# Kernel optimization log

Measured on AMD Instinct MI355X. Metric: run time of the kernel, lower is better.

## Reference

```python
import jax, jax.numpy as jnp
import numpy as np

B, S, D, F, E, K, R, H = 4, 1024, 1024, 512, 8, 2, 64, 256
TEMP = 1.0          # step=0 -> 0.5+0.5*cos(0)=1.0, clamp(min=0.1) -> 1.0
BW, EW, ZW = 0.3, 0.1, 1e-4


def fq(t):
    """Per-tensor symmetric int8 fake-quant with straight-through estimator."""
    s = jnp.maximum(jnp.max(jnp.abs(t)) / 127.0, 1e-8)
    q = jnp.clip(jnp.round(t / s), -128, 127) * s
    return t + jax.lax.stop_gradient(q - t)


def lora_lin(h, W, A, Bm):
    # base weight is frozen (requires_grad=False) and fake-quantized
    y = h @ fq(jax.lax.stop_gradient(W)).T + (h @ Bm.T) @ A.T
    return fq(y)


def ffn(h, w1, a1, b1, w2, a2, b2, w3, a3, b3):
    # use_swiglu=True path: gate = sigmoid(w3(x)); out = w2(w1(x)*gate); dropout=eval identity
    gate = jax.nn.sigmoid(lora_lin(h, w3, a3, b3))
    out = lora_lin(lora_lin(h, w1, a1, b1) * gate, w2, a2, b2)
    return fq(out)


def setup_inputs() -> dict:
    key = jax.random.key(0)
    k = jax.random.split(key, 32)
    n = lambda i, shp: jax.random.normal(k[i], shp, dtype=jnp.float32) * 0.02
    return {
        "x": jax.random.normal(k[0], (B, S, D), dtype=jnp.float32),
        "scorer_w": n(1, (E, D)), "scorer_b": jnp.zeros((E,), jnp.float32),
        "p1_w": n(2, (H, D)), "p1_b": jnp.zeros((H,), jnp.float32),
        "p2_w": n(3, (E, H)), "p2_b": jnp.zeros((E,), jnp.float32),
        "ew1_w": n(4, (E, F, D)), "ew1_a": n(5, (E, F, R)), "ew1_b": n(6, (E, R, D)),
        "ew2_w": n(7, (E, D, F)), "ew2_a": n(8, (E, D, R)), "ew2_b": n(9, (E, R, F)),
        "ew3_w": n(10, (E, F, D)), "ew3_a": n(11, (E, F, R)), "ew3_b": n(12, (E, R, D)),
        "s1_w": n(13, (F, D)), "s1_a": n(14, (F, R)), "s1_b": n(15, (R, D)),
        "s2_w": n(16, (D, F)), "s2_a": n(17, (D, R)), "s2_b": n(18, (R, F)),
        "s3_w": n(19, (F, D)), "s3_a": n(20, (F, R)), "s3_b": n(21, (R, D)),
    }


def reference(x, scorer_w, scorer_b, p1_w, p1_b, p2_w, p2_b,
              ew1_w, ew1_a, ew1_b, ew2_w, ew2_a, ew2_b, ew3_w, ew3_a, ew3_b,
              s1_w, s1_a, s1_b, s2_w, s2_a, s2_b, s3_w, s3_a, s3_b):
    xf = x.reshape(-1, D)                                           # [T, D]
    # --- router (per-token) ---
    base = (xf @ scorer_w.T + scorer_b) / TEMP                      # [T, E]
    policy = jax.nn.softmax(jax.nn.relu(xf @ p1_w.T + p1_b) @ p2_w.T + p2_b, axis=-1)
    scores = jax.nn.softmax((base + policy) * 0.5, axis=-1)         # fp32 softmax
    entropy = -(scores * jnp.log(scores + 1e-6)).sum(-1).mean()
    z_loss = ZW * (jax.nn.logsumexp(base, axis=-1) ** 2).mean()
    weights, indices = jax.lax.top_k(scores, K)                     # [T, K]
    weights = weights * TEMP
    cw = (jax.nn.one_hot(indices, E, dtype=weights.dtype) * weights[..., None]).sum(1)  # [T, E]
    usage = cw.sum(0)                                               # [E]
    uf = usage / (usage.mean() + 1e-6)
    balance_loss = BW * jnp.var(uf, ddof=1) - EW * entropy + z_loss
    # --- expert dispatch: dense masked combine (faithful to weighted scatter-add) ---
    eout = jax.vmap(lambda w1, a1, b1, w2, a2, b2, w3, a3, b3:
                    ffn(xf, w1, a1, b1, w2, a2, b2, w3, a3, b3))(
        ew1_w, ew1_a, ew1_b, ew2_w, ew2_a, ew2_b, ew3_w, ew3_a, ew3_b)  # [E, T, D]
    y = jnp.einsum('te,etd->td', cw, eout)                          # weighted combine
    z = ffn(xf, s1_w, s1_a, s1_b, s2_w, s2_a, s2_b, s3_w, s3_a, s3_b)
    out = (y + z).reshape(x.shape)
    return (out, usage, balance_loss, jnp.float32(0.0), jnp.float32(0.0))
```

## Files before the change

### kernel.cpp

```cpp
#include <hip/hip_runtime.h>

#define TTOK 4096
#define DDIM 1024
#define FDIM 512
#define NEXP 8
#define HDIM 256
#define RLORA 64
#define CROWS 14336

using u16 = unsigned short;
using f4v = __attribute__((ext_vector_type(4))) float;
using bfrag = __attribute__((ext_vector_type(8))) short;
using u16x8 = __attribute__((ext_vector_type(8))) unsigned short;

static __device__ __forceinline__ float bf2f(u16 u) {
  union { unsigned int u; float f; } x; x.u = ((unsigned int)u) << 16; return x.f;
}
static __device__ __forceinline__ u16 f2bf(float f) {
  union { float f; unsigned int u; } x; x.f = f;
  unsigned int r = (x.u + 0x7fffu + ((x.u >> 16) & 1u)) >> 16;
  return (u16)r;
}
static __device__ __forceinline__ float fq1(float t, float s) {
  float q = rintf(t / s);
  q = fminf(fmaxf(q, -128.f), 127.f);
  return q * s;
}

struct GemmGArgs {
  const u16* A; const u16* B; u16* C;
  const int* tokmap; const int2* blkmap; const int* nbrow;
};

#define STAGE1(d, kt, h) \
  __builtin_amdgcn_global_load_lds( \
    (const __attribute__((address_space(1))) void*)(gs[h] + (size_t)(kt)*64), \
    (__attribute__((address_space(3))) void*)&lds[(d)*32768 + (h)*8192 + tid*8], \
    16, 0, 0)

template <int MODE>
__global__ __launch_bounds__(1024, 4) void gemm256g(GemmGArgs g) {
  const int bid = blockIdx.x;
  const int logical = (bid & 7) * 28 + (bid >> 3);
  const int br = logical >> 2;
  if (br >= g.nbrow[0]) return;
  const int2 bm = g.blkmap[br];
  const int e = bm.x;
  const int m0 = bm.y;
  const int n0 = (logical & 3) * 256;
  const int tid = threadIdx.x;
  const int lane = tid & 63;
  const int wave = tid >> 6;
  const int wr = wave >> 2;
  const int wc = wave & 3;

  constexpr int K = MODE ? 1024 : 512;
  const u16* Bp = g.B + (size_t)e * (MODE ? 1048576 : 524288);

  __shared__ u16 lds[65536];

  const u16* gs[4];
#pragma unroll
  for (int h = 0; h < 4; h++) {
    const int row = tid >> 3, p = tid & 7;
    const int glog = p ^ (row & 7);
    const u16* basep;
    if (h < 2) {
      const int grow = m0 + h * 128 + row;
      const int t = MODE ? g.tokmap[grow] : grow;
      basep = g.A + (size_t)t * K;
    } else {
      basep = Bp + (size_t)(n0 + (h - 2) * 128 + row) * K;
    }
    gs[h] = basep + glog * 8;
  }

  f4v acc[4][4];
#pragma unroll
  for (int i = 0; i < 4; i++)
#pragma unroll
    for (int j = 0; j < 4; j++) acc[i][j] = (f4v){0.f, 0.f, 0.f, 0.f};

  const int q = lane >> 4;
  const int lx = lane & 7;
  const int l15 = lane & 15;

#pragma unroll
  for (int h = 0; h < 4; h++) STAGE1(0, 0, h);
  __syncthreads();

  constexpr int nt = K >> 6;
  for (int kt = 0; kt < nt; ++kt) {
    const int d = kt & 1;
    const int dn = d ^ 1;
    const bool more = (kt + 1 < nt);
#pragma unroll
    for (int kk = 0; kk < 2; ++kk) {
      if (more) {
        if (kk == 0) { STAGE1(dn, kt + 1, 0); STAGE1(dn, kt + 1, 1); }
        else         { STAGE1(dn, kt + 1, 2); STAGE1(dn, kt + 1, 3); }
      }
      bfrag afr[4], bfr[4];
      const int pa = ((kk * 4 + q) ^ lx) << 3;
      const int abase = d * 32768 + (wr >> 1) * 8192 + (((wr & 1) << 6) + l15) * 64 + pa;
#pragma unroll
      for (int mi = 0; mi < 4; mi++) afr[mi] = *(const bfrag*)&lds[abase + mi * 1024];
      const int bbase = d * 32768 + (2 + (wc >> 1)) * 8192 + (((wc & 1) << 6) + l15) * 64 + pa;
#pragma unroll
      for (int ni = 0; ni < 4; ni++) bfr[ni] = *(const bfrag*)&lds[bbase + ni * 1024];
      __builtin_amdgcn_s_setprio(1);
#pragma unroll
      for (int mi = 0; mi < 4; mi++)
#pragma unroll
        for (int ni = 0; ni < 4; ni++)
          acc[mi][ni] = __builtin_amdgcn_mfma_f32_16x16x32_bf16(afr[mi], bfr[ni], acc[mi][ni], 0, 0, 0);
      __builtin_amdgcn_s_setprio(0);
    }
    __syncthreads();
  }

  const int crow0 = m0 + wr * 64 + q * 4;

  if (MODE == 1) {
    u16* stage = lds;
    const int lrow0 = wr * 64 + q * 4;
    if (wc >= 2) {
      const int lc = (wc - 2) * 64 + l15;
#pragma unroll
      for (int mi = 0; mi < 4; mi++)
#pragma unroll
        for (int ni = 0; ni < 4; ni++)
#pragma unroll
          for (int r = 0; r < 4; r++)
            stage[(lrow0 + mi * 16 + r) * 136 + lc + ni * 16] = f2bf(acc[mi][ni][r]);
    }
    __syncthreads();
    if (wc < 2) {
      const int lc = wc * 64 + l15;
      const int fbase = (n0 >> 1) + lc;
#pragma unroll
      for (int mi = 0; mi < 4; mi++)
#pragma unroll
        for (int r = 0; r < 4; r++) {
          const int rowg = crow0 + mi * 16 + r;
          const int lr = lrow0 + mi * 16 + r;
#pragma unroll
          for (int ni = 0; ni < 4; ni++) {
            float y1 = acc[mi][ni][r];
            float y3 = bf2f(stage[lr * 136 + lc + ni * 16]);
            float h = y1 / (1.f + __expf(-y3));
            g.C[(size_t)rowg * FDIM + fbase + ni * 16] = f2bf(h);
          }
        }
    }
  } else {
    const int ccol0 = n0 + wc * 64 + l15;
#pragma unroll
    for (int mi = 0; mi < 4; mi++)
#pragma unroll
      for (int ni = 0; ni < 4; ni++) {
        const int col = ccol0 + ni * 16;
#pragma unroll
        for (int r = 0; r < 4; r++)
          g.C[(size_t)(crow0 + mi * 16 + r) * 1024 + col] = f2bf(acc[mi][ni][r]);
      }
  }
}

struct MidArgs {
  const u16* A64; const u16* B64; u16* C64; const float* bias64;
  const u16* A0; const u16* B0;
  const u16* Wb;
  u16* C13; u16* C2e;
  const float* amaxP;
};

__global__ __launch_bounds__(256) void mid_kernel(MidArgs g) {
  __shared__ u16 smem[25600];
  __shared__ float s_sw;
  const int bid = blockIdx.x;
  const int tid = threadIdx.x;
  const int lane = tid & 63;
  const int wave = tid >> 6;

  if (bid < 256) {
    const int wr = wave >> 1, wc = wave & 1;
    const int m0 = (bid & 63) * 64, n0 = (bid >> 6) * 64;
    const int K = DDIM, N = HDIM;
    u16* As = smem;
    u16* Bs = smem + 2048;

    const int ldrow = tid >> 2;
    const int swzcol = (((tid & 3) ^ ((tid >> 3) & 3)) << 3);
    const u16* ga = g.A64 + (size_t)(m0 + ldrow) * K + swzcol;
    const u16* gb = g.B64 + (size_t)(n0 + ldrow) * K + swzcol;

    f4v acc[2][2];
#pragma unroll
    for (int i = 0; i < 2; i++)
#pragma unroll
      for (int j = 0; j < 2; j++) acc[i][j] = (f4v){0.f, 0.f, 0.f, 0.f};

    const int rbase = lane & 15;
    const int q = lane >> 4;
    const int pg = (q ^ ((rbase >> 1) & 3)) << 3;
    const int arow = (wr << 5) + rbase;
    const int brow = (wc << 5) + rbase;

    for (int kt = 0; kt < K; kt += 32) {
      __builtin_amdgcn_global_load_lds((const __attribute__((address_space(1))) void*)(ga),
          (__attribute__((address_space(3))) void*)&As[tid * 8], 16, 0, 0);
      __builtin_amdgcn_global_load_lds((const __attribute__((address_space(1))) void*)(gb),
          (__attribute__((address_space(3))) void*)&Bs[tid * 8], 16, 0, 0);
      ga += 32; gb += 32;
      __syncthreads();
      bfrag af[2], bf[2];
#pragma unroll
      for (int mi = 0; mi < 2; mi++)
        af[mi] = *(const bfrag*)&As[(arow + mi * 16) * 32 + pg];
#pragma unroll
      for (int ni = 0; ni < 2; ni++)
        bf[ni] = *(const bfrag*)&Bs[(brow + ni * 16) * 32 + pg];
#pragma unroll
      for (int mi = 0; mi < 2; mi++)
#pragma unroll
        for (int ni = 0; ni < 2; ni++)
          acc[mi][ni] = __builtin_amdgcn_mfma_f32_16x16x32_bf16(af[mi], bf[ni], acc[mi][ni], 0, 0, 0);
      __syncthreads();
    }

    const int crow0 = m0 + (wr << 5) + ((lane >> 4) << 2);
    const int ccol0 = n0 + (wc << 5) + (lane & 15);
#pragma unroll
    for (int mi = 0; mi < 2; mi++)
#pragma unroll
      for (int ni = 0; ni < 2; ni++) {
        const int n = ccol0 + ni * 16;
        const float b = g.bias64[n];
#pragma unroll
        for (int r = 0; r < 4; r++) {
          float v = fmaxf(acc[mi][ni][r] + b, 0.f);
          g.C64[(size_t)(crow0 + mi * 16 + r) * N + n] = f2bf(v);
        }
      }
    return;
  }

  const int fid = bid - 256;
  const int z = fid >> 6;
  const int rem = fid & 63;
  const int bx = rem & 7, by = rem >> 3;
  const bool is13 = z < 18;
  if (is13 ? (bx >= 4) : (by >= 4)) return;
  const int N = is13 ? 1024 : 512;
  const int K = 64;
  const u16* Ap = is13 ? g.A0 + (size_t)z * 32768 : g.A0 + 589824 + (size_t)(z - 18) * 65536;
  const u16* Bp = is13 ? g.B0 + (size_t)z * 65536 : g.B0 + 1179648 + (size_t)(z - 18) * 32768;
  const u16* Wf = g.Wb + (size_t)z * 524288;
  u16* Cb; int flag;
  if (is13) {
    const int slot = (z >= 16) ? 8 : (z & 7);
    Cb = g.C13 + (size_t)slot * 1048576;
    flag = (z >= 8 && z < 16) || z == 17 ? 2 : 1;
  } else {
    Cb = g.C2e + (size_t)(z - 18) * 524288;
    flag = 0;
  }

  const int wr = wave >> 1, wc = wave & 1;
  const int m0 = bx * 128, n0 = by * 128;
  u16* As = smem;
  u16* Bs = smem + 4096;
  u16* stage = smem + 8192;

  if (wave == 0) {
    float m = fmaxf(g.amaxP[z * 128 + lane], g.amaxP[z * 128 + 64 + lane]);
#pragma unroll
    for (int off = 32; off > 0; off >>= 1) m = fmaxf(m, __shfl_xor(m, off));
    if (lane == 0) s_sw = fmaxf(m / 127.f, 1e-8f);
  }

  const int ldrow = tid >> 2;
  const int swzcol = (((tid & 3) ^ ((tid >> 3) & 3)) << 3);
  const u16* ga = Ap + (size_t)(m0 + ldrow) * K + swzcol;
  const u16* gb = Bp + (size_t)(n0 + ldrow) * K + swzcol;
  const size_t rowstep = (size_t)64 * K;

  f4v acc[4][4];
#pragma unroll
  for (int i = 0; i < 4; i++)
#pragma unroll
    for (int j = 0; j < 4; j++) acc[i][j] = (f4v){0.f, 0.f, 0.f, 0.f};

  const int rbase = lane & 15;
  const int q = lane >> 4;
  const int pg = (q ^ ((rbase >> 1) & 3)) << 3;
  const int arow = (wr << 6) + rbase;
  const int brow = (wc << 6) + rbase;

  for (int kt = 0; kt < K; kt += 32) {
    __builtin_amdgcn_global_load_lds((const __attribute__((address_space(1))) void*)(ga),
        (__attribute__((address_space(3))) void*)&As[tid * 8], 16, 0, 0);
    __builtin_amdgcn_global_load_lds((const __attribute__((address_space(1))) void*)(ga + rowstep),
        (__attribute__((address_space(3))) void*)&As[(256 + tid) * 8], 16, 0, 0);
    __builtin_amdgcn_global_load_lds((const __attribute__((address_space(1))) void*)(gb),
        (__attribute__((address_space(3))) void*)&Bs[tid * 8], 16, 0, 0);
    __builtin_amdgcn_global_load_lds((const __attribute__((address_space(1))) void*)(gb + rowstep),
        (__attribute__((address_space(3))) void*)&Bs[(256 + tid) * 8], 16, 0, 0);
    ga += 32; gb += 32;
    __syncthreads();
    bfrag af[4], bf[4];
#pragma unroll
    for (int mi = 0; mi < 4; mi++)
      af[mi] = *(const bfrag*)&As[(arow + mi * 16) * 32 + pg];
#pragma unroll
    for (int ni = 0; ni < 4; ni++)
      bf[ni] = *(const bfrag*)&Bs[(brow + ni * 16) * 32 + pg];
#pragma unroll
    for (int mi = 0; mi < 4; mi++)
#pragma unroll
      for (int ni = 0; ni < 4; ni++)
        acc[mi][ni] = __builtin_amdgcn_mfma_f32_16x16x32_bf16(af[mi], bf[ni], acc[mi][ni], 0, 0, 0);
    __syncthreads();
  }

  const int lrow0 = (wr << 6) + ((lane >> 4) << 2);
  const int lcol0 = (wc << 6) + (lane & 15);
#pragma unroll
  for (int mi = 0; mi < 4; mi++)
#pragma unroll
    for (int ni = 0; ni < 4; ni++) {
      const int n = lcol0 + ni * 16;
#pragma unroll
      for (int r = 0; r < 4; r++)
        stage[(lrow0 + mi * 16 + r) * 136 + n] = f2bf(acc[mi][ni][r]);
    }
  __syncthreads();
  const float sw = s_sw;

  const int dm0 = flag ? (((m0 >> 7) << 8) + (flag == 2 ? 128 : 0)) : m0;
#pragma unroll
  for (int j = 0; j < 8; j++) {
    const int s = j * 256 + tid;
    const int lr = s >> 4;
    const int n8 = (s & 15) << 3;
    const u16x8 wv = *(const u16x8*)&Wf[(size_t)(m0 + lr) * N + n0 + n8];
    const bfrag sv = *(const bfrag*)&stage[lr * 136 + n8];
    u16x8 o;
#pragma unroll
    for (int k = 0; k < 8; k++)
      o[k] = f2bf(fq1(bf2f(wv[k]), sw) + bf2f((u16)sv[k]));
    *(u16x8*)&Cb[(size_t)(dm0 + lr) * N + n0 + n8] = o;
  }
}

struct PrepArgs {
  const float* W[27]; u16* Wraw; float* amaxP;
  const float* xf; u16* xfb;
  const float* p1w; u16* p1wb;
  const float* Asrc[27]; u16* Adst;
  const float* Bsrc[27]; u16* Bdst;
};
__global__ __launch_bounds__(256) void prep_kernel(PrepArgs a) {
  const int bid = blockIdx.x;
  const int tid = threadIdx.x;
  if (bid < 3456) {
    const int t = bid >> 7;
    const int bx = bid & 127;
    const float4* src = (const float4*)a.W[t];
    ushort4* dst = (ushort4*)(a.Wraw + (size_t)t * 524288);
    const int i0 = bx * 256 + tid;
    float4 v0 = src[i0];
    float4 v1 = src[i0 + 32768];
    float4 v2 = src[i0 + 65536];
    float4 v3 = src[i0 + 98304];
    ushort4 o0, o1, o2, o3;
    o0.x = f2bf(v0.x); o0.y = f2bf(v0.y); o0.z = f2bf(v0.z); o0.w = f2bf(v0.w);
    o1.x = f2bf(v1.x); o1.y = f2bf(v1.y); o1.z = f2bf(v1.z); o1.w = f2bf(v1.w);
    o2.x = f2bf(v2.x); o2.y = f2bf(v2.y); o2.z = f2bf(v2.z); o2.w = f2bf(v2.w);
    o3.x = f2bf(v3.x); o3.y = f2bf(v3.y); o3.z = f2bf(v3.z); o3.w = f2bf(v3.w);
    dst[i0] = o0; dst[i0 + 32768] = o1; dst[i0 + 65536] = o2; dst[i0 + 98304] = o3;
    float m01 = fmaxf(fmaxf(fabsf(v0.x), fabsf(v0.y)), fmaxf(fabsf(v0.z), fabsf(v0.w)));
    float m11 = fmaxf(fmaxf(fabsf(v1.x), fabsf(v1.y)), fmaxf(fabsf(v1.z), fabsf(v1.w)));
    float m21 = fmaxf(fmaxf(fabsf(v2.x), fabsf(v2.y)), fmaxf(fabsf(v2.z), fabsf(v2.w)));
    float m31 = fmaxf(fmaxf(fabsf(v3.x), fabsf(v3.y)), fmaxf(fabsf(v3.z), fabsf(v3.w)));
    float lmax = fmaxf(fmaxf(m01, m11), fmaxf(m21, m31));
#pragma unroll
    for (int off = 32; off > 0; off >>= 1) lmax = fmaxf(lmax, __shfl_xor(lmax, off));
    __shared__ float wm[4];
    if ((tid & 63) == 0) wm[tid >> 6] = lmax;
    __syncthreads();
    if (tid == 0)
      a.amaxP[t * 128 + bx] = fmaxf(fmaxf(wm[0], wm[1]), fmaxf(wm[2], wm[3]));
    return;
  }
  const int cid = bid - 3456;
  const int slice = cid >> 10;
  const int g0 = (cid & 1023) * 256 + tid;
  const int stride = 262144;
  if (slice == 0) {
    for (int i = g0; i < 1048576; i += stride) {
      float4 v = ((const float4*)a.xf)[i];
      ushort4 o; o.x = f2bf(v.x); o.y = f2bf(v.y); o.z = f2bf(v.z); o.w = f2bf(v.w);
      ((ushort4*)a.xfb)[i] = o;
    }
  } else if (slice == 1) {
    for (int i = g0; i < 65536; i += stride) {
      float4 v = ((const float4*)a.p1w)[i];
      ushort4 o; o.x = f2bf(v.x); o.y = f2bf(v.y); o.z = f2bf(v.z); o.w = f2bf(v.w);
      ((ushort4*)a.p1wb)[i] = o;
    }
  } else if (slice == 2) {
    for (int i = g0; i < 1179648; i += stride) {
      int t, off;
      if (i < 589824) { t = i >> 15; off = i & 32767; }
      else { int j = i - 589824; t = 18 + (j >> 16); off = j & 65535; }
      a.Adst[i] = f2bf(a.Asrc[t][off]);
    }
  } else {
    for (int i = g0; i < 1474560; i += stride) {
      int t, src;
      if (i < 1179648) { t = i >> 16; int off = i & 65535; src = (off & 63) * 1024 + (off >> 6); }
      else { int j = i - 1179648; t = 18 + (j >> 15); int off = j & 32767; src = (off & 63) * 512 + (off >> 6); }
      a.Bdst[i] = f2bf(a.Bsrc[t][src]);
    }
  }
}

struct RouterArgs {
  const float* xf; const u16* ph;
  const float* sw; const float* sb;
  const float* p2w; const float* p2b;
  int* idx2; float2* wb;
  float* partials;
  int* histArr;
};
__global__ __launch_bounds__(256) void router_kernel(RouterArgs a) {
  __shared__ float sw[8][1024];
  __shared__ float p2[8][256];
  __shared__ float blog[16][8];
  __shared__ float plog[16][8];
  __shared__ int hist[8];
  const int tid = threadIdx.x;
  {
    const float4* s0 = (const float4*)a.sw;
    float4* d0 = (float4*)&sw[0][0];
    for (int i = tid; i < 2048; i += 256) d0[i] = s0[i];
    const float4* s1 = (const float4*)a.p2w;
    float4* d1 = (float4*)&p2[0][0];
    for (int i = tid; i < 512; i += 256) d1[i] = s1[i];
  }
  if (tid < 8) hist[tid] = 0;
  __syncthreads();
  const int tl = tid >> 4, s = tid & 15;
  const int token = blockIdx.x * 16 + tl;
  {
    float acc[8] = {0,0,0,0,0,0,0,0}, pacc[8] = {0,0,0,0,0,0,0,0};
    const float4* xrow = (const float4*)(a.xf + (size_t)token * 1024);
    for (int i = 0; i < 16; i++) {
      const int d4 = i * 16 + s;
      float4 xv = xrow[d4];
#pragma unroll
      for (int e = 0; e < 8; e++) {
        float4 wv = ((const float4*)&sw[e][0])[d4];
        acc[e] += xv.x * wv.x + xv.y * wv.y + xv.z * wv.z + xv.w * wv.w;
      }
    }
    const u16* phrow = a.ph + (size_t)token * 256;
    for (int i = 0; i < 16; i++) {
      const int h = i * 16 + s;
      float pv = bf2f(phrow[h]);
#pragma unroll
      for (int e = 0; e < 8; e++) pacc[e] += pv * p2[e][h];
    }
#pragma unroll
    for (int off = 8; off > 0; off >>= 1)
#pragma unroll
      for (int e = 0; e < 8; e++) {
        acc[e] += __shfl_xor(acc[e], off);
        pacc[e] += __shfl_xor(pacc[e], off);
      }
    if (s == 0) {
#pragma unroll
      for (int e = 0; e < 8; e++) {
        blog[tl][e] = acc[e] + a.sb[e];
        plog[tl][e] = pacc[e] + a.p2b[e];
      }
    }
  }
  __syncthreads();

  float vals[10];
#pragma unroll
  for (int v = 0; v < 10; v++) vals[v] = 0.f;
  if (tid < 16) {
    const int tok = blockIdx.x * 16 + tid;
    float b[8], p[8];
#pragma unroll
    for (int e = 0; e < 8; e++) { b[e] = blog[tid][e]; p[e] = plog[tid][e]; }
    float pm = p[0];
#pragma unroll
    for (int e = 1; e < 8; e++) pm = fmaxf(pm, p[e]);
    float pe[8], psum = 0.f;
#pragma unroll
    for (int e = 0; e < 8; e++) { pe[e] = expf(p[e] - pm); psum += pe[e]; }
    const float pinv = 1.f / psum;
    float sl[8];
#pragma unroll
    for (int e = 0; e < 8; e++) sl[e] = (b[e] + pe[e] * pinv) * 0.5f;
    float sm = sl[0];
#pragma unroll
    for (int e = 1; e < 8; e++) sm = fmaxf(sm, sl[e]);
    float sc[8], ssum = 0.f;
#pragma unroll
    for (int e = 0; e < 8; e++) { sc[e] = expf(sl[e] - sm); ssum += sc[e]; }
    const float sinv = 1.f / ssum;
    float ent = 0.f;
#pragma unroll
    for (int e = 0; e < 8; e++) { float v = sc[e] * sinv; sc[e] = v; ent -= v * logf(v + 1e-6f); }
    float bm = b[0];
#pragma unroll
    for (int e = 1; e < 8; e++) bm = fmaxf(bm, b[e]);
    float zs = 0.f;
#pragma unroll
    for (int e = 0; e < 8; e++) zs += expf(b[e] - bm);
    const float lse = logf(zs) + bm;
    float m1 = -1e30f, m2 = -1e30f; int i1 = 0, i2 = 0;
#pragma unroll
    for (int e = 0; e < 8; e++) {
      float v = sc[e];
      if (v > m1) { m2 = m1; i2 = i1; m1 = v; i1 = e; }
      else if (v > m2) { m2 = v; i2 = e; }
    }
    a.idx2[tok] = i1 | (i2 << 8);
    a.wb[tok] = make_float2(m1, m2);
    atomicAdd(&hist[i1], 1);
    atomicAdd(&hist[i2], 1);
    vals[0] = ent; vals[1] = lse * lse;
    vals[2 + i1] = m1; vals[2 + i2] = m2;
  }
  if (tid < 64) {
#pragma unroll
    for (int v = 0; v < 10; v++)
#pragma unroll
      for (int off = 32; off > 0; off >>= 1) vals[v] += __shfl_down(vals[v], off);
    if (tid == 0)
#pragma unroll
      for (int v = 0; v < 10; v++) a.partials[blockIdx.x * 10 + v] = vals[v];
  }
  __syncthreads();
  if (tid < 8) a.histArr[blockIdx.x * 8 + tid] = hist[tid];
}

__global__ __launch_bounds__(256) void compact_setup(const int* idx2, const int* histArr,
                                                     int2* blkmap, int* nbrow, int* tokmap,
                                                     int* posb, const float* partials, float* tail) {
  const int e = blockIdx.x;
  const int tid = threadIdx.x;
  const int lane = tid & 63, wv = tid >> 6;
  __shared__ int scnt[8];
  __shared__ int wcnt[4][8];

  {
    int local[8];
#pragma unroll
    for (int i = 0; i < 8; i++) local[i] = histArr[tid * 8 + i];
#pragma unroll
    for (int i = 0; i < 8; i++) {
      int v = local[i];
#pragma unroll
      for (int off = 32; off > 0; off >>= 1) v += __shfl_down(v, off);
      if (lane == 0) wcnt[wv][i] = v;
    }
  }
  __syncthreads();
  if (tid < 8) scnt[tid] = wcnt[0][tid] + wcnt[1][tid] + wcnt[2][tid] + wcnt[3][tid];
  __syncthreads();

  if (e == 8) {
    __shared__ float wpart[4][10];
    float pv[10];
#pragma unroll
    for (int v = 0; v < 10; v++) pv[v] = partials[tid * 10 + v];
#pragma unroll
    for (int v = 0; v < 10; v++) {
      float t = pv[v];
#pragma unroll
      for (int off = 32; off > 0; off >>= 1) t += __shfl_down(t, off);
      if (lane == 0) wpart[wv][v] = t;
    }
    __syncthreads();
    if (tid == 0) {
      float pt[10];
#pragma unroll
      for (int v = 0; v < 10; v++)
        pt[v] = wpart[0][v] + wpart[1][v] + wpart[2][v] + wpart[3][v];
      const float ent = pt[0], z = pt[1];
      float us[8];
      for (int ex = 0; ex < 8; ex++) us[ex] = pt[2 + ex];
      float tot = 0.f;
      for (int ex = 0; ex < 8; ex++) tot += us[ex];
      const float meanu = tot / 8.f;
      float uf[8], mu = 0.f;
      for (int ex = 0; ex < 8; ex++) { uf[ex] = us[ex] / (meanu + 1e-6f); mu += uf[ex]; }
      mu /= 8.f;
      float var = 0.f;
      for (int ex = 0; ex < 8; ex++) { float d = uf[ex] - mu; var += d * d; }
      var /= 7.f;
      const float bl = 0.3f * var - 0.1f * (ent / 4096.f) + 1e-4f * (z / 4096.f);
      for (int ex = 0; ex < 8; ex++) tail[ex] = us[ex];
      tail[8] = bl; tail[9] = 0.f; tail[10] = 0.f;
      int o = 0, nb = 16;
      for (int i = 0; i < 16; i++) blkmap[i] = make_int2(8, i * 256);
      for (int ex = 0; ex < 8; ex++) {
        const int nbe = (scnt[ex] + 255) >> 8;
        for (int i = 0; i < nbe; i++) blkmap[nb++] = make_int2(ex, 4096 + o + i * 256);
        o += nbe << 8;
      }
      nbrow[0] = nb;
    }
    for (int t = tid; t < 4096; t += 256) tokmap[t] = t;
    return;
  }

  __shared__ int wtot[4];
  __shared__ int carry;
  if (tid == 0) carry = 0;
  __syncthreads();
  int off = 0;
  for (int i = 0; i < e; i++) off += ((scnt[i] + 255) >> 8) << 8;
  const int base = 4096 + off;
  for (int c = 0; c < 16; c++) {
    const int t = c * 256 + tid;
    const int ii = idx2[t];
    const int i1 = ii & 255, i2 = ii >> 8;
    const int flag = (i1 == e || i2 == e) ? 1 : 0;
    const unsigned long long m = __ballot(flag);
    const int pre = __popcll(m & ((1ull << lane) - 1ull));
    if (lane == 63) wtot[wv] = pre + flag;
    __syncthreads();
    int wbase = 0;
    for (int i = 0; i < wv; i++) wbase += wtot[i];
    if (flag) {
      const int row = base + carry + wbase + pre;
      tokmap[row] = t;
      posb[t * 2 + (i2 == e ? 1 : 0)] = row;
    }
    __syncthreads();
    if (tid == 0) carry += wtot[0] + wtot[1] + wtot[2] + wtot[3];
    __syncthreads();
  }
  const int ce = scnt[e];
  const int pend = ((ce + 255) >> 8) << 8;
  for (int r = ce + tid; r < pend; r += 256) tokmap[base + r] = 0;
}

__global__ __launch_bounds__(256) void combine_g(const u16* y2c, const int* posb,
                                                 const float2* wb, float* out) {
  const int t = blockIdx.x;
  const int c = threadIdx.x;
  const float2 w = wb[t];
  const int p1 = posb[t * 2], p2 = posb[t * 2 + 1];
  ushort4 s = ((const ushort4*)(y2c + (size_t)t * 1024))[c];
  ushort4 a = ((const ushort4*)(y2c + (size_t)p1 * 1024))[c];
  ushort4 b = ((const ushort4*)(y2c + (size_t)p2 * 1024))[c];
  float4 o;
  o.x = bf2f(s.x) + w.x * bf2f(a.x) + w.y * bf2f(b.x);
  o.y = bf2f(s.y) + w.x * bf2f(a.y) + w.y * bf2f(b.y);
  o.z = bf2f(s.z) + w.x * bf2f(a.z) + w.y * bf2f(b.z);
  o.w = bf2f(s.w) + w.x * bf2f(a.w) + w.y * bf2f(b.w);
  ((float4*)(out + (size_t)t * 1024))[c] = o;
}

extern "C" void kernel_launch(void* const* d_in, const int* in_sizes, int n_in,
                              void* d_out, int out_size, void* d_ws, size_t ws_size,
                              hipStream_t stream) {
  const float* x = (const float*)d_in[0];
  const float* scorer_w = (const float*)d_in[1];
  const float* scorer_b = (const float*)d_in[2];
  const float* p1_w = (const float*)d_in[3];
  const float* p1_b = (const float*)d_in[4];
  const float* p2_w = (const float*)d_in[5];
  const float* p2_b = (const float*)d_in[6];
  const float* ew1_w = (const float*)d_in[7];
  const float* ew1_a = (const float*)d_in[8];
  const float* ew1_b = (const float*)d_in[9];
  const float* ew2_w = (const float*)d_in[10];
  const float* ew2_a = (const float*)d_in[11];
  const float* ew2_b = (const float*)d_in[12];
  const float* ew3_w = (const float*)d_in[13];
  const float* ew3_a = (const float*)d_in[14];
  const float* ew3_b = (const float*)d_in[15];
  const float* s1_w = (const float*)d_in[16];
  const float* s1_a = (const float*)d_in[17];
  const float* s1_b = (const float*)d_in[18];
  const float* s2_w = (const float*)d_in[19];
  const float* s2_a = (const float*)d_in[20];
  const float* s2_b = (const float*)d_in[21];
  const float* s3_w = (const float*)d_in[22];
  const float* s3_a = (const float*)d_in[23];
  const float* s3_b = (const float*)d_in[24];
  float* outf = (float*)d_out;

  char* w = (char*)d_ws;
  auto alloc = [&](size_t bytes) { char* p = w; w += (bytes + 255) & ~(size_t)255; return p; };
  u16* xfb  = (u16*)alloc((size_t)TTOK * DDIM * 2);
  u16* ph   = (u16*)alloc((size_t)TTOK * HDIM * 2);
  u16* p1wb = (u16*)alloc((size_t)HDIM * DDIM * 2);
  u16* Adst = (u16*)alloc((size_t)1179648 * 2);
  u16* Bdst = (u16*)alloc((size_t)1474560 * 2);
  u16* Wraw = (u16*)alloc((size_t)27 * 524288 * 2);
  u16* W13  = (u16*)alloc((size_t)9 * 1024 * 1024 * 2);
  u16* W2e  = (u16*)alloc((size_t)9 * 1024 * 512 * 2);
  u16* h2c  = (u16*)alloc((size_t)CROWS * FDIM * 2);
  u16* y2c  = (u16*)alloc((size_t)CROWS * DDIM * 2);
  float* partials = (float*)alloc(256 * 10 * 4);
  float* amaxP = (float*)alloc(27 * 128 * 4);
  int* histArr = (int*)alloc(256 * 8 * 4);
  int2* blkmap = (int2*)alloc(64 * 8);
  int* nbrow  = (int*)alloc(4);
  int* tokmap = (int*)alloc(CROWS * 4);
  int* posb   = (int*)alloc(TTOK * 2 * 4);
  int* idx2   = (int*)alloc(TTOK * 4);
  float2* wb  = (float2*)alloc(TTOK * 8);

  {
    PrepArgs a{};
    for (int e = 0; e < 8; e++) {
      a.W[e] = ew1_w + (size_t)e * 524288;
      a.W[8 + e] = ew3_w + (size_t)e * 524288;
      a.W[18 + e] = ew2_w + (size_t)e * 524288;
      a.Asrc[e] = ew1_a + (size_t)e * 32768;
      a.Asrc[8 + e] = ew3_a + (size_t)e * 32768;
      a.Asrc[18 + e] = ew2_a + (size_t)e * 65536;
      a.Bsrc[e] = ew1_b + (size_t)e * 65536;
      a.Bsrc[8 + e] = ew3_b + (size_t)e * 65536;
      a.Bsrc[18 + e] = ew2_b + (size_t)e * 32768;
    }
    a.W[16] = s1_w; a.W[17] = s3_w; a.W[26] = s2_w;
    a.Asrc[16] = s1_a; a.Asrc[17] = s3_a; a.Asrc[26] = s2_a;
    a.Bsrc[16] = s1_b; a.Bsrc[17] = s3_b; a.Bsrc[26] = s2_b;
    a.Wraw = Wraw; a.amaxP = amaxP;
    a.xf = x; a.xfb = xfb; a.p1w = p1_w; a.p1wb = p1wb;
    a.Adst = Adst; a.Bdst = Bdst;
    hipLaunchKernelGGL(prep_kernel, dim3(7552), dim3(256), 0, stream, a);
  }
  {
    MidArgs g{};
    g.A64 = xfb; g.B64 = p1wb; g.C64 = ph; g.bias64 = p1_b;
    g.A0 = Adst; g.B0 = Bdst; g.Wb = Wraw; g.C13 = W13; g.C2e = W2e; g.amaxP = amaxP;
    hipLaunchKernelGGL(mid_kernel, dim3(1984), dim3(256), 0, stream, g);
  }
  {
    RouterArgs r{};
    r.xf = x; r.ph = ph; r.sw = scorer_w; r.sb = scorer_b;
    r.p2w = p2_w; r.p2b = p2_b;
    r.idx2 = idx2; r.wb = wb; r.partials = partials; r.histArr = histArr;
    hipLaunchKernelGGL(router_kernel, dim3(256), dim3(256), 0, stream, r);
  }
  hipLaunchKernelGGL(compact_setup, dim3(9), dim3(256), 0, stream,
                     idx2, histArr, blkmap, nbrow, tokmap, posb, partials,
                     outf + (size_t)TTOK * DDIM);
  {
    GemmGArgs g{xfb, W13, h2c, tokmap, blkmap, nbrow};
    hipLaunchKernelGGL(gemm256g<1>, dim3(224), dim3(1024), 0, stream, g);
  }
  {
    GemmGArgs g{h2c, W2e, y2c, tokmap, blkmap, nbrow};
    hipLaunchKernelGGL(gemm256g<0>, dim3(224), dim3(1024), 0, stream, g);
  }
  hipLaunchKernelGGL(combine_g, dim3(4096), dim3(256), 0, stream, y2c, posb, wb, outf);
}
```

Before: 147.5 us.

## Shrink grouped expert GEMM tiles from 256x256 to 128x128 for more blocks

Replaces the 1024-thread 256x256-tile grouped GEMM with a 256-thread 128x128-tile version, launching four times as many blocks so the 256 CUs get better occupancy and load balance. The W1/W3 interleaving produced by the mid kernel changes from 128-row to 64-row granularity so that each 128-column output tile still holds matching gate and up halves for the fused sigmoid epilogue. The cost is lower per-block data reuse and more global traffic for the A and B operands.

```diff
diff --git a/kernel.cpp b/kernel.cpp
--- a/kernel.cpp
+++ b/kernel.cpp
@@ -32,48 +32,52 @@
   const int* tokmap; const int2* blkmap; const int* nbrow;
 };
 
-#define STAGE1(d, kt, h) \
+#define STG(d, kt, h, l) \
   __builtin_amdgcn_global_load_lds( \
-    (const __attribute__((address_space(1))) void*)(gs[h] + (size_t)(kt)*64), \
-    (__attribute__((address_space(3))) void*)&lds[(d)*32768 + (h)*8192 + tid*8], \
+    (const __attribute__((address_space(1))) void*)(gs[(h)*4+(l)] + (size_t)(kt)*64), \
+    (__attribute__((address_space(3))) void*)&lds[(d)*16384 + (h)*8192 + (tid + (l)*256)*8], \
     16, 0, 0)
 
 template <int MODE>
-__global__ __launch_bounds__(1024, 4) void gemm256g(GemmGArgs g) {
+__global__ __launch_bounds__(256, 2) void gemm128g(GemmGArgs g) {
   const int bid = blockIdx.x;
-  const int logical = (bid & 7) * 28 + (bid >> 3);
-  const int br = logical >> 2;
+  const int logical = (bid & 7) * 112 + (bid >> 3);
+  const int br = logical >> 4;
   if (br >= g.nbrow[0]) return;
   const int2 bm = g.blkmap[br];
   const int e = bm.x;
-  const int m0 = bm.y;
-  const int n0 = (logical & 3) * 256;
+  const int sub = logical & 15;
+  const int m0 = bm.y + (sub >> 3) * 128;
+  const int n0 = (sub & 7) * 128;
   const int tid = threadIdx.x;
   const int lane = tid & 63;
   const int wave = tid >> 6;
-  const int wr = wave >> 2;
-  const int wc = wave & 3;
+  const int wr = wave >> 1;
+  const int wc = wave & 1;
 
   constexpr int K = MODE ? 1024 : 512;
   const u16* Bp = g.B + (size_t)e * (MODE ? 1048576 : 524288);
 
-  __shared__ u16 lds[65536];
-
-  const u16* gs[4];
-#pragma unroll
-  for (int h = 0; h < 4; h++) {
-    const int row = tid >> 3, p = tid & 7;
-    const int glog = p ^ (row & 7);
-    const u16* basep;
-    if (h < 2) {
-      const int grow = m0 + h * 128 + row;
-      const int t = MODE ? g.tokmap[grow] : grow;
-      basep = g.A + (size_t)t * K;
-    } else {
-      basep = Bp + (size_t)(n0 + (h - 2) * 128 + row) * K;
-    }
-    gs[h] = basep + glog * 8;
-  }
+  __shared__ u16 lds[32768];
+
+  const u16* gs[8];
+#pragma unroll
+  for (int h = 0; h < 2; h++)
+#pragma unroll
+    for (int l = 0; l < 4; l++) {
+      const int slot = tid + l * 256;
+      const int row = slot >> 3, p = slot & 7;
+      const int glog = p ^ (row & 7);
+      const u16* basep;
+      if (h == 0) {
+        const int grow = m0 + row;
+        const int t = MODE ? g.tokmap[grow] : grow;
+        basep = g.A + (size_t)t * K;
+      } else {
+        basep = Bp + (size_t)(n0 + row) * K;
+      }
+      gs[h * 4 + l] = basep + glog * 8;
+    }
 
   f4v acc[4][4];
 #pragma unroll
@@ -86,7 +90,9 @@
   const int l15 = lane & 15;
 
 #pragma unroll
-  for (int h = 0; h < 4; h++) STAGE1(0, 0, h);
+  for (int h = 0; h < 2; h++)
+#pragma unroll
+    for (int l = 0; l < 4; l++) STG(0, 0, h, l);
   __syncthreads();
 
   constexpr int nt = K >> 6;
@@ -97,15 +103,17 @@
 #pragma unroll
     for (int kk = 0; kk < 2; ++kk) {
       if (more) {
-        if (kk == 0) { STAGE1(dn, kt + 1, 0); STAGE1(dn, kt + 1, 1); }
-        else         { STAGE1(dn, kt + 1, 2); STAGE1(dn, kt + 1, 3); }
+        if (kk == 0) { STG(dn, kt + 1, 0, 0); STG(dn, kt + 1, 0, 1);
+                       STG(dn, kt + 1, 0, 2); STG(dn, kt + 1, 0, 3); }
+        else         { STG(dn, kt + 1, 1, 0); STG(dn, kt + 1, 1, 1);
+                       STG(dn, kt + 1, 1, 2); STG(dn, kt + 1, 1, 3); }
       }
       bfrag afr[4], bfr[4];
       const int pa = ((kk * 4 + q) ^ lx) << 3;
-      const int abase = d * 32768 + (wr >> 1) * 8192 + (((wr & 1) << 6) + l15) * 64 + pa;
+      const int abase = d * 16384 + (wr * 64 + l15) * 64 + pa;
 #pragma unroll
       for (int mi = 0; mi < 4; mi++) afr[mi] = *(const bfrag*)&lds[abase + mi * 1024];
-      const int bbase = d * 32768 + (2 + (wc >> 1)) * 8192 + (((wc & 1) << 6) + l15) * 64 + pa;
+      const int bbase = d * 16384 + 8192 + (wc * 64 + l15) * 64 + pa;
 #pragma unroll
       for (int ni = 0; ni < 4; ni++) bfr[ni] = *(const bfrag*)&lds[bbase + ni * 1024];
       __builtin_amdgcn_s_setprio(1);
@@ -120,24 +128,22 @@
   }
 
   const int crow0 = m0 + wr * 64 + q * 4;
+  const int lrow0 = wr * 64 + q * 4;
 
   if (MODE == 1) {
     u16* stage = lds;
-    const int lrow0 = wr * 64 + q * 4;
-    if (wc >= 2) {
-      const int lc = (wc - 2) * 64 + l15;
+    if (wc == 1) {
 #pragma unroll
       for (int mi = 0; mi < 4; mi++)
 #pragma unroll
         for (int ni = 0; ni < 4; ni++)
 #pragma unroll
           for (int r = 0; r < 4; r++)
-            stage[(lrow0 + mi * 16 + r) * 136 + lc + ni * 16] = f2bf(acc[mi][ni][r]);
-    }
-    __syncthreads();
-    if (wc < 2) {
-      const int lc = wc * 64 + l15;
-      const int fbase = (n0 >> 1) + lc;
+            stage[(lrow0 + mi * 16 + r) * 72 + ni * 16 + l15] = f2bf(acc[mi][ni][r]);
+    }
+    __syncthreads();
+    if (wc == 0) {
+      const int fbase = (n0 >> 1) + l15;
 #pragma unroll
       for (int mi = 0; mi < 4; mi++)
 #pragma unroll
@@ -147,7 +153,7 @@
 #pragma unroll
           for (int ni = 0; ni < 4; ni++) {
             float y1 = acc[mi][ni][r];
-            float y3 = bf2f(stage[lr * 136 + lc + ni * 16]);
+            float y3 = bf2f(stage[lr * 72 + ni * 16 + l15]);
             float h = y1 / (1.f + __expf(-y3));
             g.C[(size_t)rowg * FDIM + fbase + ni * 16] = f2bf(h);
           }
@@ -338,19 +344,20 @@
   __syncthreads();
   const float sw = s_sw;
 
-  const int dm0 = flag ? (((m0 >> 7) << 8) + (flag == 2 ? 128 : 0)) : m0;
 #pragma unroll
   for (int j = 0; j < 8; j++) {
     const int s = j * 256 + tid;
     const int lr = s >> 4;
     const int n8 = (s & 15) << 3;
-    const u16x8 wv = *(const u16x8*)&Wf[(size_t)(m0 + lr) * N + n0 + n8];
+    const int m = m0 + lr;
+    const int dm = flag ? (((m >> 6) << 7) + (m & 63) + (flag == 2 ? 64 : 0)) : m;
+    const u16x8 wv = *(const u16x8*)&Wf[(size_t)m * N + n0 + n8];
     const bfrag sv = *(const bfrag*)&stage[lr * 136 + n8];
     u16x8 o;
 #pragma unroll
     for (int k = 0; k < 8; k++)
       o[k] = f2bf(fq1(bf2f(wv[k]), sw) + bf2f((u16)sv[k]));
-    *(u16x8*)&Cb[(size_t)(dm0 + lr) * N + n0 + n8] = o;
+    *(u16x8*)&Cb[(size_t)dm * N + n0 + n8] = o;
   }
 }
 
@@ -763,11 +770,11 @@
                      outf + (size_t)TTOK * DDIM);
   {
     GemmGArgs g{xfb, W13, h2c, tokmap, blkmap, nbrow};
-    hipLaunchKernelGGL(gemm256g<1>, dim3(224), dim3(1024), 0, stream, g);
+    hipLaunchKernelGGL(gemm128g<1>, dim3(896), dim3(256), 0, stream, g);
   }
   {
     GemmGArgs g{h2c, W2e, y2c, tokmap, blkmap, nbrow};
-    hipLaunchKernelGGL(gemm256g<0>, dim3(224), dim3(1024), 0, stream, g);
+    hipLaunchKernelGGL(gemm128g<0>, dim3(896), dim3(256), 0, stream, g);
   }
   hipLaunchKernelGGL(combine_g, dim3(4096), dim3(256), 0, stream, y2c, posb, wb, outf);
 }
```

After: 151.5 us. +2.7%, slower.
